# Performance work log

Measured on AMD Instinct MI355X. Metric: run time of the kernel, lower is better.

Reference implementation:

```python
import jax, jax.numpy as jnp
import numpy as np

B, CH_IN, D, H, W = 8, 256, 64, 16, 16
S = CH_IN // 2  # shurink = 128


def setup_inputs() -> dict:
    key = jax.random.key(0)
    ks = jax.random.split(key, 9)
    kstd = (2.0 / CH_IN) ** 0.5   # kaiming-like for 1x1 conv, fan_in = CH_IN
    ostd = (2.0 / S) ** 0.5
    x = jax.random.normal(ks[0], (B, CH_IN, D, H, W), dtype=jnp.float32)
    wk = jax.random.normal(ks[1], (S, CH_IN), dtype=jnp.float32) * kstd
    wq = jax.random.normal(ks[2], (S, CH_IN), dtype=jnp.float32) * kstd
    wv = jax.random.normal(ks[3], (S, CH_IN), dtype=jnp.float32) * kstd
    wo = jax.random.normal(ks[4], (CH_IN, S), dtype=jnp.float32) * ostd
    bk = jax.random.normal(ks[5], (S,), dtype=jnp.float32) * 0.01
    bq = jax.random.normal(ks[6], (S,), dtype=jnp.float32) * 0.01
    bv = jax.random.normal(ks[7], (S,), dtype=jnp.float32) * 0.01
    bo = jax.random.normal(ks[8], (CH_IN,), dtype=jnp.float32) * 0.01
    return {"x": x, "wk": wk, "bk": bk, "wq": wq, "bq": bq,
            "wv": wv, "bv": bv, "wo": wo, "bo": bo}


def reference(x, wk, bk, wq, bq, wv, bv, wo, bo):
    # 1x1x1 Conv3d == channel contraction: [B,C,D,H,W] x [S,C] -> [B,S,D,H,W]
    def proj(w, b):
        return jnp.einsum('bcdhw,oc->bodhw', x, w) + b[None, :, None, None, None]

    k = proj(wk, bk)  # [B,S,D,H,W]
    q = proj(wq, bq)
    v = proj(wv, bv)
    s_dim = k.shape[1]
    scale = 1.0 / jnp.sqrt(jnp.asarray(s_dim, x.dtype))
    # torch: bmm(k^T, q) over per-(b,h,w) [S,D] matrices -> [D_i, D_j]
    scores = jnp.einsum('bsihw,bsjhw->bhwij', k, q) * scale  # [B,H,W,D,D]
    # torch softmax(dim=1) on [BHW, D, D] == softmax over i (keys axis)
    a = jax.nn.softmax(scores, axis=3)
    # torch: bmm(v, a) -> [S, D_j]
    att = jnp.einsum('bsihw,bhwij->bsjhw', v, a)  # [B,S,D,H,W]
    out = jnp.einsum('bsdhw,cs->bcdhw', att, wo) + bo[None, :, None, None, None]
    return x + out  # atten_factor = 1
```

## Files before the change

kernel.cpp:

```cpp
#include <hip/hip_runtime.h>
#include <hip/hip_bf16.h>


typedef __bf16 bf16_t;
typedef bf16_t bf16x8 __attribute__((ext_vector_type(8)));
typedef bf16_t bf16x4 __attribute__((ext_vector_type(4)));
typedef float  f32x4  __attribute__((ext_vector_type(4)));

#define NB   8
#define NC   256
#define ND   64
#define NHW  256
#define NS   128

#define MFMA16 __builtin_amdgcn_mfma_f32_16x16x32_bf16

__device__ __forceinline__ int swz(int row, int col) {
  return col ^ ((row & 7) << 3);
}

__device__ __forceinline__ bf16x8 pack8(float4 a, float4 b) {
  bf16x8 r;
  r[0] = (bf16_t)a.x; r[1] = (bf16_t)a.y; r[2] = (bf16_t)a.z; r[3] = (bf16_t)a.w;
  r[4] = (bf16_t)b.x; r[5] = (bf16_t)b.y; r[6] = (bf16_t)b.z; r[7] = (bf16_t)b.w;
  return r;
}

__device__ __forceinline__ bf16x8 ldg_w8(const float* p) {
  float4 a = *(const float4*)p;
  float4 b = *(const float4*)(p + 4);
  return pack8(a, b);
}

__global__ __launch_bounds__(256) void transpose_x_w(
    const float* __restrict__ x,
    const float* __restrict__ wk, const float* __restrict__ wq,
    const float* __restrict__ wv, const float* __restrict__ wo,
    bf16_t* __restrict__ xT, bf16_t* __restrict__ wsW) {
  __shared__ bf16_t tile[64 * 72];
  const int bid = blockIdx.x;
  if (bid >= 8192) {
    const int wid = bid - 8192;
    const int mat = wid >> 3, sub = wid & 7;
    const int t = threadIdx.x;
    if (mat < 3) {
      const float* src = (mat == 0) ? wk : (mat == 1) ? wq : wv;
      bf16_t* dst = wsW + mat * 32768;
      int s = sub * 16 + (t >> 4), c0 = (t & 15) * 16;
      const float* p = src + s * NC + c0;
      float4 a0 = *(const float4*)p, a1 = *(const float4*)(p + 4);
      float4 a2 = *(const float4*)(p + 8), a3 = *(const float4*)(p + 12);
      *(bf16x8*)(dst + (c0 >> 3) * 1024 + s * 8)       = pack8(a0, a1);
      *(bf16x8*)(dst + ((c0 >> 3) + 1) * 1024 + s * 8) = pack8(a2, a3);
    } else {
      bf16_t* dst = wsW + 98304;
      int c = sub * 32 + (t >> 3), sc0 = (t & 7) * 16;
      const float* p = wo + c * NS + sc0;
      float4 a0 = *(const float4*)p, a1 = *(const float4*)(p + 4);
      float4 a2 = *(const float4*)(p + 8), a3 = *(const float4*)(p + 12);
      *(bf16x8*)(dst + (sc0 >> 3) * 2048 + c * 8)       = pack8(a0, a1);
      *(bf16x8*)(dst + ((sc0 >> 3) + 1) * 2048 + c * 8) = pack8(a2, a3);
    }
    return;
  }
  const int ct = bid & 3, hwt = (bid >> 2) & 3;
  const int d = (bid >> 4) & 63, b = bid >> 10;
  const int c0 = ct * 64, hw0 = hwt * 64;
  const int t = threadIdx.x;
  const int hwq = t & 15, chi = t >> 4;

  #pragma unroll
  for (int q = 0; q < 4; ++q) {
    int c = q * 16 + chi;
    float4 v4 = *(const float4*)(x + ((size_t)((b * NC + c0 + c) * ND + d)) * NHW + hw0 + hwq * 4);
    tile[(hwq * 4 + 0) * 72 + c] = (bf16_t)v4.x;
    tile[(hwq * 4 + 1) * 72 + c] = (bf16_t)v4.y;
    tile[(hwq * 4 + 2) * 72 + c] = (bf16_t)v4.z;
    tile[(hwq * 4 + 3) * 72 + c] = (bf16_t)v4.w;
  }
  __syncthreads();
  #pragma unroll
  for (int i = 0; i < 2; ++i) {
    int idx = t + 256 * i;
    int hw = idx >> 3, q = idx & 7;
    bf16x8 v8 = *(const bf16x8*)&tile[hw * 72 + q * 8];
    *(bf16x8*)(xT + ((size_t)((b * ND + d) * NHW + hw0 + hw)) * NC + c0 + q * 8) = v8;
  }
}

__global__ __launch_bounds__(256, 3) void qkv_attn3(
    const bf16_t* __restrict__ xT, const bf16_t* __restrict__ wsW,
    const float* __restrict__ bk, const float* __restrict__ bq,
    const float* __restrict__ bv, bf16_t* __restrict__ att) {
  __shared__ bf16_t lds[24576];
  bf16_t* kT   = lds;
  bf16_t* qT   = lds + 8192;
  bf16_t* vS   = lds + 16384;
  bf16_t* xTl  = lds;
  bf16_t* aT   = lds;
  bf16_t* attT = lds + 8192;

  const int gid = blockIdx.x;
  const int b = gid & 7, hw = gid >> 3;
  const int t = threadIdx.x, w = t >> 6, lane = t & 63;
  const int l16 = lane & 15, q4 = lane >> 4;

  const int mat = w >> 1;
  const int sb = (w & 1) * 64;
  const bf16_t* wm = mat ? (wsW + 32768) : wsW;
  const bf16_t* wvF = wsW + 65536;
  const float* bm = mat ? bq : bk;
  bf16_t* dstKQ = mat ? qT : kT;
  const int sbv = w * 32;

  f32x4 acc[4][4] = {};
  f32x4 accv[4][2] = {};

  for (int cc = 0; cc < 2; ++cc) {
    __syncthreads();
    #pragma unroll
    for (int jj = 0; jj < 4; ++jj) {
      int id = jj * 256 + t;
      int d = id >> 4, cg = (id & 15) * 8;
      bf16x8 v8 = *(const bf16x8*)(xT + ((size_t)((b * ND + d) * NHW + hw)) * NC + cc * 128 + cg);
      *(bf16x8*)&xTl[d * 128 + swz(d, cg)] = v8;
    }
    __syncthreads();
    #pragma unroll
    for (int ks = 0; ks < 4; ++ks) {
      const int kb = ks * 32 + q4 * 8;
      const int kgf = ((cc * 128 + kb) >> 3) * 1024;
      bf16x8 xfr[4], afk[4], bfv[2];
      #pragma unroll
      for (int i = 0; i < 4; ++i) {
        int row = i * 16 + l16;
        xfr[i] = *(const bf16x8*)&xTl[row * 128 + swz(row, kb)];
        int s = sb + i * 16 + l16;
        afk[i] = *(const bf16x8*)(wm + kgf + s * 8);
      }
      #pragma unroll
      for (int i = 0; i < 2; ++i) {
        int s = sbv + i * 16 + l16;
        bfv[i] = *(const bf16x8*)(wvF + kgf + s * 8);
      }
      #pragma unroll
      for (int nt = 0; nt < 4; ++nt)
        #pragma unroll
        for (int mt = 0; mt < 4; ++mt)
          acc[mt][nt] = MFMA16(afk[mt], xfr[nt], acc[mt][nt], 0, 0, 0);
      #pragma unroll
      for (int nt = 0; nt < 2; ++nt)
        #pragma unroll
        for (int mt = 0; mt < 4; ++mt)
          accv[mt][nt] = MFMA16(xfr[mt], bfv[nt], accv[mt][nt], 0, 0, 0);
    }
  }
  __syncthreads();

  #pragma unroll
  for (int mt = 0; mt < 4; ++mt) {
    int s0 = sb + mt * 16 + q4 * 4;
    float4 b4 = *(const float4*)(bm + s0);
    #pragma unroll
    for (int nt = 0; nt < 4; ++nt) {
      int d = nt * 16 + l16;
      bf16x4 pk;
      pk[0] = (bf16_t)(acc[mt][nt][0] + b4.x);
      pk[1] = (bf16_t)(acc[mt][nt][1] + b4.y);
      pk[2] = (bf16_t)(acc[mt][nt][2] + b4.z);
      pk[3] = (bf16_t)(acc[mt][nt][3] + b4.w);
      *(bf16x4*)&dstKQ[d * NS + swz(d, s0)] = pk;
    }
  }
  #pragma unroll
  for (int nt = 0; nt < 2; ++nt) {
    int s = sbv + nt * 16 + l16;
    float bvs = bv[s];
    #pragma unroll
    for (int mt = 0; mt < 4; ++mt) {
      int d0 = mt * 16 + q4 * 4;
      bf16x4 pv;
      pv[0] = (bf16_t)(accv[mt][nt][0] + bvs);
      pv[1] = (bf16_t)(accv[mt][nt][1] + bvs);
      pv[2] = (bf16_t)(accv[mt][nt][2] + bvs);
      pv[3] = (bf16_t)(accv[mt][nt][3] + bvs);
      *(bf16x4*)&vS[s * ND + (d0 ^ ((s & 7) << 3))] = pv;
    }
  }
  __syncthreads();

  float ps[16];
  {
    f32x4 sacc[4] = {};
    for (int ks = 0; ks < 4; ++ks) {
      const int kb = ks * 32 + q4 * 8;
      int jrow = w * 16 + l16;
      bf16x8 bfr = *(const bf16x8*)&qT[jrow * NS + swz(jrow, kb)];
      #pragma unroll
      for (int it = 0; it < 4; ++it) {
        int irow = it * 16 + l16;
        bf16x8 afr = *(const bf16x8*)&kT[irow * NS + swz(irow, kb)];
        sacc[it] = MFMA16(afr, bfr, sacc[it], 0, 0, 0);
      }
    }
    const float scale = 0.088388347648318447f;
    float mx = -1e30f;
    #pragma unroll
    for (int it = 0; it < 4; ++it)
      #pragma unroll
      for (int r = 0; r < 4; ++r) {
        float vv = sacc[it][r] * scale;
        ps[it * 4 + r] = vv;
        mx = fmaxf(mx, vv);
      }
    mx = fmaxf(mx, __shfl_xor(mx, 16));
    mx = fmaxf(mx, __shfl_xor(mx, 32));
    float sum = 0.f;
    #pragma unroll
    for (int i = 0; i < 16; ++i) { ps[i] = __expf(ps[i] - mx); sum += ps[i]; }
    sum += __shfl_xor(sum, 16);
    sum += __shfl_xor(sum, 32);
    float inv = 1.f / sum;
    #pragma unroll
    for (int i = 0; i < 16; ++i) ps[i] *= inv;
  }
  __syncthreads();

  {
    int j = w * 16 + l16;
    #pragma unroll
    for (int it = 0; it < 4; ++it) {
      bf16x4 pk;
      #pragma unroll
      for (int r = 0; r < 4; ++r) pk[r] = (bf16_t)ps[it * 4 + r];
      *(bf16x4*)&aT[j * ND + ((it * 16 + q4 * 4) ^ ((j & 7) << 3))] = pk;
    }
  }
  __syncthreads();

  {
    const int sbp = w * 32;
    f32x4 pacc[2][4] = {};
    #pragma unroll
    for (int ki = 0; ki < 2; ++ki) {
      const int kb = ki * 32 + q4 * 8;
      bf16x8 afr[2];
      #pragma unroll
      for (int mt = 0; mt < 2; ++mt) {
        int srow = sbp + mt * 16 + l16;
        afr[mt] = *(const bf16x8*)&vS[srow * ND + (kb ^ ((srow & 7) << 3))];
      }
      #pragma unroll
      for (int nt = 0; nt < 4; ++nt) {
        int jrow = nt * 16 + l16;
        bf16x8 bfr = *(const bf16x8*)&aT[jrow * ND + (kb ^ ((jrow & 7) << 3))];
        #pragma unroll
        for (int mt = 0; mt < 2; ++mt)
          pacc[mt][nt] = MFMA16(afr[mt], bfr, pacc[mt][nt], 0, 0, 0);
      }
    }
    #pragma unroll
    for (int nt = 0; nt < 4; ++nt) {
      int j = nt * 16 + l16;
      #pragma unroll
      for (int mt = 0; mt < 2; ++mt) {
        bf16x4 pk;
        #pragma unroll
        for (int r = 0; r < 4; ++r) pk[r] = (bf16_t)pacc[mt][nt][r];
        *(bf16x4*)&attT[j * NS + swz(j, sbp + mt * 16 + q4 * 4)] = pk;
      }
    }
  }
  __syncthreads();

  #pragma unroll
  for (int jj = 0; jj < 4; ++jj) {
    int f = jj * 2048 + t * 8;
    int d = f >> 7, s0 = f & 127;
    bf16x8 v8 = *(const bf16x8*)&attT[d * NS + (s0 ^ ((d & 7) << 3))];
    *(bf16x8*)(att + ((size_t)((b * ND + d) * NHW + hw)) * NS + s0) = v8;
  }
}

__global__ __launch_bounds__(256, 4) void out_proj3(
    const bf16_t* __restrict__ att_ws,
    const bf16_t* __restrict__ woF, const float* __restrict__ bo,
    const float* __restrict__ x, float* __restrict__ out) {
  __shared__ union {
    bf16_t slab[128 * 128];
    float  stage[64 * 132];
  } sm;
  const int bid = blockIdx.x;
  const int ht = bid & 7, dcq = (bid >> 3) & 15, ch = (bid >> 7) & 1, b = bid >> 8;
  const int t = threadIdx.x, w = t >> 6, lane = t & 63;
  const int l16 = lane & 15, g = lane >> 4;
  const int mh = w >> 1, nh = w & 1;

  {
    const int j = t & 15;
    const int r0 = t >> 4;
    #pragma unroll
    for (int pp = 0; pp < 8; ++pp) {
      int row = pp * 16 + r0;
      int d = row >> 5, hw = row & 31;
      bf16x8 v8 = *(const bf16x8*)(att_ws +
          ((size_t)((b * ND + dcq * 4 + d) * NHW + ht * 32 + hw)) * NS + j * 8);
      *(bf16x8*)&sm.slab[row * NS + ((j ^ (hw & 7)) << 3)] = v8;
    }
  }
  __syncthreads();

  f32x4 acc[4][4] = {};
  #pragma unroll
  for (int kq = 0; kq < 4; ++kq) {
    bf16x8 af[4];
    #pragma unroll
    for (int mt = 0; mt < 4; ++mt) {
      int c = ch * 128 + mh * 64 + mt * 16 + l16;
      af[mt] = *(const bf16x8*)(woF + (kq * 4 + g) * 2048 + c * 8);
    }
    #pragma unroll
    for (int nt = 0; nt < 4; ++nt) {
      int row = nh * 64 + nt * 16 + l16;
      int hwl = row & 31;
      bf16x8 bfr = *(const bf16x8*)&sm.slab[row * NS + (((kq * 4 + g) ^ (hwl & 7)) << 3)];
      #pragma unroll
      for (int mt = 0; mt < 4; ++mt)
        acc[mt][nt] = MFMA16(af[mt], bfr, acc[mt][nt], 0, 0, 0);
    }
  }

  #pragma unroll
  for (int p = 0; p < 2; ++p) {
    __syncthreads();
    if (mh == p) {
      #pragma unroll
      for (int mt = 0; mt < 4; ++mt) {
        #pragma unroll
        for (int nt = 0; nt < 4; ++nt) {
          int row = nh * 64 + nt * 16 + l16;
          int dl = row >> 5;
          int hws = (row & 31) ^ (g << 3);
          int base = (mt * 16 + g * 4) * 132 + dl * 32 + hws;
          #pragma unroll
          for (int r = 0; r < 4; ++r)
            sm.stage[base + r * 132] = acc[mt][nt][r];
        }
      }
    }
    __syncthreads();
    #pragma unroll
    for (int ii = 0; ii < 8; ++ii) {
      int c6 = ii * 8 + w * 2 + (lane >> 5);
      int c = ch * 128 + p * 64 + c6;
      int dq = (lane >> 3) & 3;
      int hw4 = (lane & 7) * 4;
      float4 v = *(const float4*)&sm.stage[c6 * 132 + dq * 32 + (hw4 ^ (((c6 >> 2) & 3) << 3))];
      size_t gi = ((size_t)(b * NC + c) * ND + dcq * 4 + dq) * NHW + ht * 32 + hw4;
      float4 xv = *(const float4*)(x + gi);
      float bias = bo[c];
      float4 o;
      o.x = v.x + bias + xv.x;
      o.y = v.y + bias + xv.y;
      o.z = v.z + bias + xv.z;
      o.w = v.w + bias + xv.w;
      *(float4*)(out + gi) = o;
    }
  }
}

struct SMemF {
  union {
    bf16_t xT[ND * NC];
    struct { bf16_t aT[ND * ND]; bf16_t attT[ND * NS]; } p2;
  } u;
  bf16_t kT[ND * NS];
  bf16_t qT[ND * NS];
  bf16_t vS[NS * ND];
};

__global__ __launch_bounds__(256) void attn_fused(
    const float* __restrict__ x,
    const float* __restrict__ wk, const float* __restrict__ bk,
    const float* __restrict__ wq, const float* __restrict__ bq,
    const float* __restrict__ wv, const float* __restrict__ bv,
    const float* __restrict__ wo, const float* __restrict__ bo,
    float* __restrict__ out) {
  __shared__ SMemF sm;
  const int gid = blockIdx.x;
  const int b = gid & 7;
  const int hw = gid >> 3;
  const int t = threadIdx.x;
  const int w = t >> 6;
  const int lane = t & 63;
  const int l16 = lane & 15;
  const int q4 = lane >> 4;
  const float* xb = x + (size_t)b * NC * ND * NHW + hw;
  {
    const int d = t & 63;
    const int cb = (t >> 6) * 64;
    for (int jj = 0; jj < 8; ++jj) {
      bf16x8 pk;
      #pragma unroll
      for (int e = 0; e < 8; ++e) {
        int c = cb + jj * 8 + e;
        pk[e] = (bf16_t)xb[(size_t)(c * ND + d) * NHW];
      }
      *(bf16x8*)&sm.u.xT[d * NC + swz(d, cb + jj * 8)] = pk;
    }
  }
  __syncthreads();
  {
    const int mat = w >> 1;
    const int sb = (w & 1) * 64;
    const float* wm = mat ? wq : wk;
    const float* bm = mat ? bq : bk;
    bf16_t* dst = mat ? sm.qT : sm.kT;
    f32x4 acc[4][4] = {};
    for (int ks = 0; ks < 8; ++ks) {
      const int kb = ks * 32 + q4 * 8;
      bf16x8 afr[4];
      #pragma unroll
      for (int mt = 0; mt < 4; ++mt) {
        int row = mt * 16 + l16;
        afr[mt] = *(const bf16x8*)&sm.u.xT[row * NC + swz(row, kb)];
      }
      #pragma unroll
      for (int st = 0; st < 4; ++st) {
        int s = sb + st * 16 + l16;
        bf16x8 bfr = ldg_w8(wm + s * NC + kb);
        #pragma unroll
        for (int mt = 0; mt < 4; ++mt)
          acc[mt][st] = MFMA16(afr[mt], bfr, acc[mt][st], 0, 0, 0);
      }
    }
    #pragma unroll
    for (int st = 0; st < 4; ++st) {
      int s = sb + st * 16 + l16;
      float bias = bm[s];
      #pragma unroll
      for (int mt = 0; mt < 4; ++mt) {
        #pragma unroll
        for (int r = 0; r < 4; ++r) {
          int d = mt * 16 + q4 * 4 + r;
          dst[d * NS + swz(d, s)] = (bf16_t)(acc[mt][st][r] + bias);
        }
      }
    }
  }
  {
    const int sb = w * 32;
    f32x4 acc[2][4] = {};
    for (int ks = 0; ks < 8; ++ks) {
      const int kb = ks * 32 + q4 * 8;
      bf16x8 afr[2];
      #pragma unroll
      for (int mt = 0; mt < 2; ++mt)
        afr[mt] = ldg_w8(wv + (sb + mt * 16 + l16) * NC + kb);
      #pragma unroll
      for (int nt = 0; nt < 4; ++nt) {
        int row = nt * 16 + l16;
        bf16x8 bfr = *(const bf16x8*)&sm.u.xT[row * NC + swz(row, kb)];
        #pragma unroll
        for (int mt = 0; mt < 2; ++mt)
          acc[mt][nt] = MFMA16(afr[mt], bfr, acc[mt][nt], 0, 0, 0);
      }
    }
    #pragma unroll
    for (int mt = 0; mt < 2; ++mt) {
      #pragma unroll
      for (int r = 0; r < 4; ++r) {
        int s = sb + mt * 16 + q4 * 4 + r;
        float bias = bv[s];
        #pragma unroll
        for (int nt = 0; nt < 4; ++nt) {
          int d = nt * 16 + l16;
          sm.vS[s * ND + swz(s, d)] = (bf16_t)(acc[mt][nt][r] + bias);
        }
      }
    }
  }
  __syncthreads();
  {
    f32x4 sacc[4] = {};
    for (int ks = 0; ks < 4; ++ks) {
      const int kb = ks * 32 + q4 * 8;
      int jrow = w * 16 + l16;
      bf16x8 bfr = *(const bf16x8*)&sm.qT[jrow * NS + swz(jrow, kb)];
      #pragma unroll
      for (int it = 0; it < 4; ++it) {
        int irow = it * 16 + l16;
        bf16x8 afr = *(const bf16x8*)&sm.kT[irow * NS + swz(irow, kb)];
        sacc[it] = MFMA16(afr, bfr, sacc[it], 0, 0, 0);
      }
    }
    const float scale = 0.088388347648318447f;
    float ps[16];
    float mx = -1e30f;
    #pragma unroll
    for (int it = 0; it < 4; ++it) {
      #pragma unroll
      for (int r = 0; r < 4; ++r) {
        float vv = sacc[it][r] * scale;
        ps[it * 4 + r] = vv;
        mx = fmaxf(mx, vv);
      }
    }
    mx = fmaxf(mx, __shfl_xor(mx, 16));
    mx = fmaxf(mx, __shfl_xor(mx, 32));
    float sum = 0.f;
    #pragma unroll
    for (int i = 0; i < 16; ++i) { ps[i] = __expf(ps[i] - mx); sum += ps[i]; }
    sum += __shfl_xor(sum, 16);
    sum += __shfl_xor(sum, 32);
    float inv = 1.f / sum;
    int j = w * 16 + l16;
    #pragma unroll
    for (int it = 0; it < 4; ++it) {
      bf16x4 pk;
      #pragma unroll
      for (int r = 0; r < 4; ++r) pk[r] = (bf16_t)(ps[it * 4 + r] * inv);
      *(bf16x4*)&sm.u.p2.aT[j * ND + swz(j, it * 16 + q4 * 4)] = pk;
    }
  }
  __syncthreads();
  {
    const int sb = w * 32;
    f32x4 acc[2][4] = {};
    #pragma unroll
    for (int ki = 0; ki < 2; ++ki) {
      const int kb = ki * 32 + q4 * 8;
      bf16x8 afr[2];
      #pragma unroll
      for (int mt = 0; mt < 2; ++mt) {
        int srow = sb + mt * 16 + l16;
        afr[mt] = *(const bf16x8*)&sm.vS[srow * ND + swz(srow, kb)];
      }
      #pragma unroll
      for (int nt = 0; nt < 4; ++nt) {
        int jrow = nt * 16 + l16;
        bf16x8 bfr = *(const bf16x8*)&sm.u.p2.aT[jrow * ND + swz(jrow, kb)];
        #pragma unroll
        for (int mt = 0; mt < 2; ++mt)
          acc[mt][nt] = MFMA16(afr[mt], bfr, acc[mt][nt], 0, 0, 0);
      }
    }
    #pragma unroll
    for (int nt = 0; nt < 4; ++nt) {
      int j = nt * 16 + l16;
      #pragma unroll
      for (int mt = 0; mt < 2; ++mt) {
        bf16x4 pk;
        #pragma unroll
        for (int r = 0; r < 4; ++r) pk[r] = (bf16_t)acc[mt][nt][r];
        *(bf16x4*)&sm.u.p2.attT[j * NS + swz(j, sb + mt * 16 + q4 * 4)] = pk;
      }
    }
  }
  __syncthreads();
  {
    const int cb = w * 64;
    f32x4 acc[4][4] = {};
    for (int ks = 0; ks < 4; ++ks) {
      const int kb = ks * 32 + q4 * 8;
      bf16x8 afr[4];
      #pragma unroll
      for (int mt = 0; mt < 4; ++mt)
        afr[mt] = ldg_w8(wo + (cb + mt * 16 + l16) * NS + kb);
      #pragma unroll
      for (int nt = 0; nt < 4; ++nt) {
        int jrow = nt * 16 + l16;
        bf16x8 bfr = *(const bf16x8*)&sm.u.p2.attT[jrow * NS + swz(jrow, kb)];
        #pragma unroll
        for (int mt = 0; mt < 4; ++mt)
          acc[mt][nt] = MFMA16(afr[mt], bfr, acc[mt][nt], 0, 0, 0);
      }
    }
    #pragma unroll
    for (int mt = 0; mt < 4; ++mt) {
      #pragma unroll
      for (int r = 0; r < 4; ++r) {
        int c = cb + mt * 16 + q4 * 4 + r;
        float bias = bo[c];
        #pragma unroll
        for (int nt = 0; nt < 4; ++nt) {
          int d = nt * 16 + l16;
          size_t gi = (size_t)(((b * NC + c) * ND + d) * NHW + hw);
          out[gi] = acc[mt][nt][r] + bias + x[gi];
        }
      }
    }
  }
}

extern "C" void kernel_launch(void* const* d_in, const int* in_sizes, int n_in,
                              void* d_out, int out_size, void* d_ws, size_t ws_size,
                              hipStream_t stream) {
  const float* x  = (const float*)d_in[0];
  const float* wk = (const float*)d_in[1];
  const float* bk = (const float*)d_in[2];
  const float* wq = (const float*)d_in[3];
  const float* bq = (const float*)d_in[4];
  const float* wv = (const float*)d_in[5];
  const float* bv = (const float*)d_in[6];
  const float* wo = (const float*)d_in[7];
  const float* bo = (const float*)d_in[8];
  float* out = (float*)d_out;

  const size_t need = (size_t)(131072 + 33554432 + 16777216) * 2;
  if (ws_size >= need) {
    bf16_t* wsW = (bf16_t*)d_ws;
    bf16_t* xT  = wsW + 131072;
    bf16_t* att = xT + 33554432;
    transpose_x_w<<<dim3(8224), dim3(256), 0, stream>>>(x, wk, wq, wv, wo, xT, wsW);
    qkv_attn3<<<dim3(2048), dim3(256), 0, stream>>>(xT, wsW, bk, bq, bv, att);
    out_proj3<<<dim3(2048), dim3(256), 0, stream>>>(att, wsW + 98304, bo, x, out);
  } else {
    attn_fused<<<dim3(2048), dim3(256), 0, stream>>>(x, wk, bk, wq, bq, wv, bv, wo, bo, out);
  }
}
```

Baseline: 134.5 us.

## Split out-projection over four channel quarters and prefetch residual before staging

```diff
diff --git a/kernel.cpp b/kernel.cpp
--- a/kernel.cpp
+++ b/kernel.cpp
@@ -282,7 +282,7 @@
   }
 }
 
-__global__ __launch_bounds__(256, 4) void out_proj3(
+__global__ __launch_bounds__(256, 4) void out_proj4(
     const bf16_t* __restrict__ att_ws,
     const bf16_t* __restrict__ woF, const float* __restrict__ bo,
     const float* __restrict__ x, float* __restrict__ out) {
@@ -291,7 +291,7 @@
     float  stage[64 * 132];
   } sm;
   const int bid = blockIdx.x;
-  const int ht = bid & 7, dcq = (bid >> 3) & 15, ch = (bid >> 7) & 1, b = bid >> 8;
+  const int ht = bid & 7, dcq = (bid >> 3) & 15, cq = (bid >> 7) & 3, b = bid >> 9;
   const int t = threadIdx.x, w = t >> 6, lane = t & 63;
   const int l16 = lane & 15, g = lane >> 4;
   const int mh = w >> 1, nh = w & 1;
@@ -310,13 +310,13 @@
   }
   __syncthreads();
 
-  f32x4 acc[4][4] = {};
+  f32x4 acc[2][4] = {};
   #pragma unroll
   for (int kq = 0; kq < 4; ++kq) {
-    bf16x8 af[4];
-    #pragma unroll
-    for (int mt = 0; mt < 4; ++mt) {
-      int c = ch * 128 + mh * 64 + mt * 16 + l16;
+    bf16x8 af[2];
+    #pragma unroll
+    for (int mt = 0; mt < 2; ++mt) {
+      int c = cq * 64 + mh * 32 + mt * 16 + l16;
       af[mt] = *(const bf16x8*)(woF + (kq * 4 + g) * 2048 + c * 8);
     }
     #pragma unroll
@@ -325,47 +325,52 @@
       int hwl = row & 31;
       bf16x8 bfr = *(const bf16x8*)&sm.slab[row * NS + (((kq * 4 + g) ^ (hwl & 7)) << 3)];
       #pragma unroll
-      for (int mt = 0; mt < 4; ++mt)
+      for (int mt = 0; mt < 2; ++mt)
         acc[mt][nt] = MFMA16(af[mt], bfr, acc[mt][nt], 0, 0, 0);
     }
   }
 
-  #pragma unroll
-  for (int p = 0; p < 2; ++p) {
-    __syncthreads();
-    if (mh == p) {
-      #pragma unroll
-      for (int mt = 0; mt < 4; ++mt) {
-        #pragma unroll
-        for (int nt = 0; nt < 4; ++nt) {
-          int row = nh * 64 + nt * 16 + l16;
-          int dl = row >> 5;
-          int hws = (row & 31) ^ (g << 3);
-          int base = (mt * 16 + g * 4) * 132 + dl * 32 + hws;
-          #pragma unroll
-          for (int r = 0; r < 4; ++r)
-            sm.stage[base + r * 132] = acc[mt][nt][r];
-        }
-      }
-    }
-    __syncthreads();
-    #pragma unroll
-    for (int ii = 0; ii < 8; ++ii) {
-      int c6 = ii * 8 + w * 2 + (lane >> 5);
-      int c = ch * 128 + p * 64 + c6;
-      int dq = (lane >> 3) & 3;
-      int hw4 = (lane & 7) * 4;
-      float4 v = *(const float4*)&sm.stage[c6 * 132 + dq * 32 + (hw4 ^ (((c6 >> 2) & 3) << 3))];
-      size_t gi = ((size_t)(b * NC + c) * ND + dcq * 4 + dq) * NHW + ht * 32 + hw4;
-      float4 xv = *(const float4*)(x + gi);
-      float bias = bo[c];
-      float4 o;
-      o.x = v.x + bias + xv.x;
-      o.y = v.y + bias + xv.y;
-      o.z = v.z + bias + xv.z;
-      o.w = v.w + bias + xv.w;
-      *(float4*)(out + gi) = o;
-    }
+  float4 xv[8];
+  size_t gis[8];
+  #pragma unroll
+  for (int ii = 0; ii < 8; ++ii) {
+    int c6 = ii * 8 + w * 2 + (lane >> 5);
+    int c = cq * 64 + c6;
+    int dq = (lane >> 3) & 3;
+    int hw4 = (lane & 7) * 4;
+    gis[ii] = ((size_t)(b * NC + c) * ND + dcq * 4 + dq) * NHW + ht * 32 + hw4;
+    xv[ii] = *(const float4*)(x + gis[ii]);
+  }
+
+  __syncthreads();
+  #pragma unroll
+  for (int mt = 0; mt < 2; ++mt) {
+    #pragma unroll
+    for (int nt = 0; nt < 4; ++nt) {
+      int row = nh * 64 + nt * 16 + l16;
+      int dl = row >> 5;
+      int hws = (row & 31) ^ (g << 3);
+      int base = (mh * 32 + mt * 16 + g * 4) * 132 + dl * 32 + hws;
+      #pragma unroll
+      for (int r = 0; r < 4; ++r)
+        sm.stage[base + r * 132] = acc[mt][nt][r];
+    }
+  }
+  __syncthreads();
+  #pragma unroll
+  for (int ii = 0; ii < 8; ++ii) {
+    int c6 = ii * 8 + w * 2 + (lane >> 5);
+    int c = cq * 64 + c6;
+    int dq = (lane >> 3) & 3;
+    int hw4 = (lane & 7) * 4;
+    float4 v = *(const float4*)&sm.stage[c6 * 132 + dq * 32 + (hw4 ^ (((c6 >> 2) & 3) << 3))];
+    float bias = bo[c];
+    float4 o;
+    o.x = v.x + bias + xv[ii].x;
+    o.y = v.y + bias + xv[ii].y;
+    o.z = v.z + bias + xv[ii].z;
+    o.w = v.w + bias + xv[ii].w;
+    *(float4*)(out + gis[ii]) = o;
   }
 }
 
@@ -614,7 +619,7 @@
     bf16_t* att = xT + 33554432;
     transpose_x_w<<<dim3(8224), dim3(256), 0, stream>>>(x, wk, wq, wv, wo, xT, wsW);
     qkv_attn3<<<dim3(2048), dim3(256), 0, stream>>>(xT, wsW, bk, bq, bv, att);
-    out_proj3<<<dim3(2048), dim3(256), 0, stream>>>(att, wsW + 98304, bo, x, out);
+    out_proj4<<<dim3(4096), dim3(256), 0, stream>>>(att, wsW + 98304, bo, x, out);
   } else {
     attn_fused<<<dim3(2048), dim3(256), 0, stream>>>(x, wk, bk, wq, bq, wv, bv, wo, bo, out);
   }
```

New measurement: 131.6 us, median of 2. 2.2% less time.
